# Optimization experiments

Hardware: AMD Instinct MI355X
Metric: run time of the kernel (lower is better)

Reference implementation:

```python
import jax, jax.numpy as jnp
import numpy as np

N_AGENTS = 10000
N_TARGETS = 10000
N_EDGES = 320000
IN_CH = 8
DS = 32          # n_channels // 2 per GAT preprocessor
NCH = 64         # n_channels
C = 128          # 2 * n_channels hidden width
OUT = 2
N_TAPS = 3
N_LAYERS = 2
RADIUS = 2.0
K_NBR = 10       # max_num_neighbors in radius_graph
BIG = 1e9


def radius_nbrs(qpos, kpos, radius, k, exclude_self):
    """For each query point, indices of <=k nearest key points within radius."""
    d2 = jnp.sum((qpos[:, None, :] - kpos[None, :, :]) ** 2, axis=-1)  # [Nq, Nk]
    if exclude_self:
        n = qpos.shape[0]
        d2 = d2.at[jnp.arange(n), jnp.arange(n)].set(BIG)
    d2 = jnp.where(d2 <= radius * radius, d2, BIG)
    negv, idx = jax.lax.top_k(-d2, k)   # nearest-k (deterministic stand-in for PyG's first-k)
    valid = negv > -BIG * 0.5           # [Nq, k] True where a real in-radius neighbor
    return idx, valid


def gatv2(src_feats, dst_feats, idx, valid, Wl, Wr, att, b):
    """Single-head GATv2Conv over a fixed-K neighbor list (idx indexes src_feats)."""
    xl = src_feats @ Wl                      # [Ns, H] messages
    xr = dst_feats @ Wr                      # [Nd, H]
    g = jax.nn.leaky_relu(xl[idx] + xr[:, None, :], 0.2)   # [Nd, K, H]
    s = jnp.einsum('nkh,h->nk', g, att)
    s = jnp.where(valid, s, -BIG)
    s = s - jnp.max(s, axis=1, keepdims=True)
    p = jnp.exp(s) * valid                   # masked exp; isolated nodes -> all-zero
    alpha = p / (jnp.sum(p, axis=1, keepdims=True) + 1e-16)
    return jnp.einsum('nk,nkh->nh', alpha, xl[idx]) + b


def graph_filter(x, src, dst, W, b, n):
    """Polynomial graph filter: y = sum_k S^k x W_k + b, S = unweighted adjacency."""
    y = x @ W[0]
    h = x
    for k in range(1, W.shape[0]):
        h = jax.ops.segment_sum(h[src], dst, num_segments=n)  # one shift tap
        y = y + h @ W[k]
    return y + b


def setup_inputs() -> dict:
    key = jax.random.key(0)
    ks = jax.random.split(key, 16)
    f32 = jnp.float32
    return {
        'own_obs': jax.random.normal(ks[0], (N_AGENTS, IN_CH), dtype=f32),
        'agent_positions': jax.random.uniform(ks[1], (N_AGENTS, 2), dtype=f32) * 100.0,
        'target_positions': jax.random.uniform(ks[2], (N_TARGETS, 2), dtype=f32) * 100.0,
        'W_self': jax.random.normal(ks[3], (IN_CH, NCH), dtype=f32) * 0.1,
        'b_self': jnp.zeros((NCH,), f32),
        'ag_Wl': jax.random.normal(ks[4], (2, DS), dtype=f32) * 0.1,
        'ag_Wr': jax.random.normal(ks[5], (2, DS), dtype=f32) * 0.1,
        'ag_att': jax.random.normal(ks[6], (DS,), dtype=f32) * 0.1,
        'ag_b': jnp.zeros((DS,), f32),
        'tg_Wl': jax.random.normal(ks[7], (2, DS), dtype=f32) * 0.1,
        'tg_Wr': jax.random.normal(ks[8], (2, DS), dtype=f32) * 0.1,
        'tg_att': jax.random.normal(ks[9], (DS,), dtype=f32) * 0.1,
        'tg_b': jnp.zeros((DS,), f32),
        'gf_W': jax.random.normal(ks[10], (N_LAYERS, N_TAPS + 1, C, C), dtype=f32) * (1.0 / np.sqrt(C)),
        'gf_b': jnp.zeros((N_LAYERS, C), f32),
        'bn_gamma': jnp.ones((N_LAYERS, C), f32),
        'bn_beta': jnp.zeros((N_LAYERS, C), f32),
        'W_read': jax.random.normal(ks[11], (C, OUT), dtype=f32) * 0.1,
        'b_read': jnp.zeros((OUT,), f32),
        'edge_index': jax.random.randint(ks[12], (2, N_EDGES), 0, N_AGENTS, dtype=jnp.int32),
    }


def reference(own_obs, agent_positions, target_positions, W_self, b_self,
              ag_Wl, ag_Wr, ag_att, ag_b, tg_Wl, tg_Wr, tg_att, tg_b,
              gf_W, gf_b, bn_gamma, bn_beta, W_read, b_read, edge_index):
    n = agent_positions.shape[0]
    # dynamic radius graphs (agent-agent; target->agent)
    a_idx, a_valid = radius_nbrs(agent_positions, agent_positions, RADIUS, K_NBR, True)
    t_idx, t_valid = radius_nbrs(agent_positions, target_positions, RADIUS, K_NBR, False)

    s = own_obs @ W_self + b_self                                            # self MLP (1 layer)
    a = gatv2(agent_positions, agent_positions, a_idx, a_valid, ag_Wl, ag_Wr, ag_att, ag_b)
    t = gatv2(target_positions, agent_positions, t_idx, t_valid, tg_Wl, tg_Wr, tg_att, tg_b)
    x = jnp.concatenate([s, a, t], axis=1)                                   # [N, 128]

    src, dst = edge_index[0], edge_index[1]
    for l in range(N_LAYERS):
        h = graph_filter(x, src, dst, gf_W[l], gf_b[l], n)
        mu = jnp.mean(h, axis=0)
        var = jnp.var(h, axis=0)
        h = (h - mu) / jnp.sqrt(var + 1e-5) * bn_gamma[l] + bn_beta[l]       # BatchNorm
        x = x + jax.nn.leaky_relu(h, 0.01)                                   # residual block
    return x @ W_read + b_read
```

## Files before the change

### kernel.cpp

```cpp
#include <hip/hip_runtime.h>

typedef unsigned long long u64;
typedef unsigned int u32;
typedef unsigned short ushort_t;

#define NA 10000
#define NE 320000
#define KN 10
#define GRID 50
#define NCELL (GRID * GRID)

typedef __attribute__((ext_vector_type(8))) short short8v;
typedef __attribute__((ext_vector_type(4))) float f32x4;

__device__ __forceinline__ u32 f2bf(float f) {
  union { float f; u32 u; } v; v.f = f;
  return (v.u + 0x7fffu + ((v.u >> 16) & 1u)) >> 16;
}
__device__ __forceinline__ float bf2f(u32 b) {
  union { u32 u; float f; } v; v.u = b << 16;
  return v.f;
}

__device__ __forceinline__ void insert10(u64* top, u64 key) {
#pragma unroll
  for (int t = 9; t > 0; --t) {
    u64 prev = top[t - 1];
    u64 cur = top[t];
    top[t] = (key < prev) ? prev : ((key < cur) ? key : cur);
  }
  top[0] = (key < top[0]) ? key : top[0];
}

__device__ __forceinline__ int cell_of(float2 p) {
  int cx = (int)(p.x * 0.5f);
  int cy = (int)(p.y * 0.5f);
  cx = min(max(cx, 0), GRID - 1);
  cy = min(max(cy, 0), GRID - 1);
  return cy * GRID + cx;
}

__global__ __launch_bounds__(256) void k_zero_packw(int* __restrict__ deg, int* __restrict__ cur,
                                                    int* __restrict__ chist, int* __restrict__ ccur,
                                                    int* __restrict__ dcur,
                                                    const float* __restrict__ gfW,
                                                    ushort_t* __restrict__ Wh, ushort_t* __restrict__ Wlo) {
  int i = blockIdx.x * 256 + threadIdx.x;
  if (i < NA) deg[i] = 0;
  else if (i < 2 * NA) cur[i - NA] = 0;
  else if (i < 2 * NA + 2 * NCELL) chist[i - 2 * NA] = 0;
  else if (i < 2 * NA + 4 * NCELL) ccur[i - 2 * NA - 2 * NCELL] = 0;
  else if (i < 2 * NA + 4 * NCELL + 128) dcur[i - 2 * NA - 4 * NCELL] = 0;
  if (i < 131072) {
    int l = i >> 16;
    int rem = i & 65535;
    int t = rem >> 14;
    int k = (rem >> 7) & 127;
    int n = rem & 127;
    float v = gfW[(size_t)i];
    int kt = k >> 5;
    int hi = (k >> 3) & 3;
    int j = k & 7;
    int ct = n >> 4;
    int lane = hi * 16 + (n & 15);
    size_t dst = (((((size_t)(l * 4 + t) * 4 + kt) * 8 + ct) * 64 + lane) * 8 + j);
    u32 h = f2bf(v);
    float r = v - bf2f(h);
    Wh[dst] = (ushort_t)h;
    Wlo[dst] = (ushort_t)f2bf(r);
  }
}

__global__ __launch_bounds__(256) void k_hist_self(const int* __restrict__ edst,
                                                   const float2* __restrict__ apos,
                                                   const float2* __restrict__ tpos,
                                                   int* __restrict__ deg, int* __restrict__ chist,
                                                   const float* __restrict__ own_obs,
                                                   const float* __restrict__ W_self, const float* __restrict__ b_self,
                                                   float* __restrict__ x) {
  __shared__ float sW[512], sb[64];
  int t = threadIdx.x;
  for (int i = t; i < 512; i += 256) sW[i] = W_self[i];
  if (t < 64) sb[t] = b_self[t];
  __syncthreads();
  int i = blockIdx.x * 256 + t;
  if (i < NE) {
    atomicAdd(&deg[edst[i]], 1);
  } else if (i < NE + 2 * NA) {
    int ii = i - NE;
    int graph = (ii >= NA) ? 1 : 0;
    int idx = ii - graph * NA;
    float2 p = graph ? tpos[idx] : apos[idx];
    atomicAdd(&chist[graph * NCELL + cell_of(p)], 1);
  } else if (i < NE + 2 * NA + 8 * NA) {
    int gid = i - NE - 2 * NA;
    int q = gid >> 3;
    int c8 = (gid & 7) * 8;
    const float4* op = (const float4*)(own_obs + (size_t)q * 8);
    float4 o0 = op[0], o1 = op[1];
    float obs[8] = {o0.x, o0.y, o0.z, o0.w, o1.x, o1.y, o1.z, o1.w};
    float out[8];
#pragma unroll
    for (int jj = 0; jj < 8; ++jj) {
      int c = c8 + jj;
      float s = sb[c];
#pragma unroll
      for (int k = 0; k < 8; ++k) s += obs[k] * sW[k * 64 + c];
      out[jj] = s;
    }
    float* xrow = x + (size_t)q * 128 + c8;
    *(float4*)(xrow) = make_float4(out[0], out[1], out[2], out[3]);
    *(float4*)(xrow + 4) = make_float4(out[4], out[5], out[6], out[7]);
  }
}

__global__ __launch_bounds__(1024) void k_scan_all(const int* __restrict__ deg, int* __restrict__ rp,
                                                   const int* __restrict__ chist, int* __restrict__ crp,
                                                   int* __restrict__ dbase) {
  int t = threadIdx.x;
  if (blockIdx.x == 2) {
    __shared__ int dh[128];
    if (t < 128) dh[t] = 0;
    __syncthreads();
    for (int i = t; i < NA; i += 1024) atomicAdd(&dh[min(deg[i], 127)], 1);
    __syncthreads();
    if (t == 0) {
      int run = 0;
      for (int b = 0; b < 128; ++b) { int c = dh[b]; dbase[b] = run; run += c; }
    }
    return;
  }
  __shared__ int part[1024];
  const int* in;
  int* out;
  int per, tot;
  if (blockIdx.x == 0) { in = deg; out = rp; per = 10; tot = NA; }
  else { in = chist; out = crp; per = 5; tot = 2 * NCELL; }
  int beg = min(t * per, tot), end = min(beg + per, tot);
  int s = 0;
  for (int i = beg; i < end; ++i) s += in[i];
  part[t] = s;
  __syncthreads();
  for (int o = 1; o < 1024; o <<= 1) {
    int v = part[t];
    int u = (t >= o) ? part[t - o] : 0;
    __syncthreads();
    part[t] = v + u;
    __syncthreads();
  }
  int base = (t > 0) ? part[t - 1] : 0;
  for (int i = beg; i < end; ++i) { out[i] = base; base += in[i]; }
  if (t == 1023) out[tot] = part[1023];
}

__global__ __launch_bounds__(256) void k_scatter_all(const int* __restrict__ esrc, const int* __restrict__ edst,
                                                     const int* __restrict__ rp, int* __restrict__ cur,
                                                     int* __restrict__ col,
                                                     const float2* __restrict__ apos, const float2* __restrict__ tpos,
                                                     const int* __restrict__ crp, int* __restrict__ ccur,
                                                     float2* __restrict__ ps, int* __restrict__ pid,
                                                     const int* __restrict__ deg, const int* __restrict__ dbase,
                                                     int* __restrict__ dcur, int* __restrict__ perm) {
  int i = blockIdx.x * 256 + threadIdx.x;
  if (i < NE) {
    int d = edst[i];
    int p = atomicAdd(&cur[d], 1);
    col[rp[d] + p] = esrc[i];
  } else if (i < NE + 2 * NA) {
    int ii = i - NE;
    int graph = (ii >= NA) ? 1 : 0;
    int idx = ii - graph * NA;
    float2 p = graph ? tpos[idx] : apos[idx];
    int gc = graph * NCELL + cell_of(p);
    int o = crp[gc] + atomicAdd(&ccur[gc], 1);
    ps[o] = p;
    pid[o] = idx;
  } else if (i < NE + 2 * NA + NA) {
    int r = i - NE - 2 * NA;
    int b = min(deg[r], 127);
    int pos = atomicAdd(&dcur[b], 1);
    perm[dbase[b] + pos] = r;
  }
}

__global__ __launch_bounds__(256) void k_nbr_gat(const float2* __restrict__ apos, const float2* __restrict__ tpos,
                                                 const int* __restrict__ crp,
                                                 const float2* __restrict__ ps, const int* __restrict__ pid,
                                                 const float* __restrict__ agWl, const float* __restrict__ agWr,
                                                 const float* __restrict__ agatt, const float* __restrict__ agb,
                                                 const float* __restrict__ tgWl, const float* __restrict__ tgWr,
                                                 const float* __restrict__ tgatt, const float* __restrict__ tgb,
                                                 float* __restrict__ x) {
  __shared__ float sWl[2][64], sWr[2][64], satt[2][32], sbb[2][32];
  int t = threadIdx.x;
  if (t < 64) { sWl[0][t] = agWl[t]; sWr[0][t] = agWr[t]; sWl[1][t] = tgWl[t]; sWr[1][t] = tgWr[t]; }
  else if (t < 96) {
    int u = t - 64;
    satt[0][u] = agatt[u]; sbb[0][u] = agb[u]; satt[1][u] = tgatt[u]; sbb[1][u] = tgb[u];
  }
  __syncthreads();
  int tid = blockIdx.x * 256 + t;
  if (tid >= 2 * NA) return;
  int graph = (tid >= NA) ? 1 : 0;
  int q = tid - graph * NA;
  float2 qp = apos[q];
  int cx = min(max((int)(qp.x * 0.5f), 0), GRID - 1);
  int cy = min(max((int)(qp.y * 0.5f), 0), GRID - 1);

  u64 top[10];
#pragma unroll
  for (int k = 0; k < 10; ++k) top[k] = ~0ull;

  int x0 = max(cx - 1, 0), x1 = min(cx + 1, GRID - 1);
  int y0 = max(cy - 1, 0), y1 = min(cy + 1, GRID - 1);
  for (int yy = y0; yy <= y1; ++yy) {
    int cb = graph * NCELL + yy * GRID + x0;
    int ce = graph * NCELL + yy * GRID + x1;
    int b = crp[cb], e = crp[ce + 1];
    for (int j = b; j < e; ++j) {
      float2 kp = ps[j];
      float dx = qp.x - kp.x;
      float dy = qp.y - kp.y;
      float d2 = __fadd_rn(__fmul_rn(dx, dx), __fmul_rn(dy, dy));
      int g = pid[j];
      if (d2 <= 4.0f && !(graph == 0 && g == q)) {
        u64 key = ((u64)__float_as_uint(d2) << 32) | (u32)g;
        if (key < top[9]) insert10(top, key);
      }
    }
  }
  int cnt = 0;
#pragma unroll
  for (int k = 0; k < 10; ++k) cnt += (top[k] != ~0ull) ? 1 : 0;
  int idx[10];
#pragma unroll
  for (int k = 0; k < 10; ++k) idx[k] = (k < cnt) ? (int)(u32)(top[k] & 0xffffffffu) : 0;

  const float2* srcpos = graph ? tpos : apos;
  const float* wl = sWl[graph];
  const float* wr = sWr[graph];
  const float* at = satt[graph];
  const float* bb = sbb[graph];
  float xr[32];
#pragma unroll
  for (int c = 0; c < 32; ++c) xr[c] = qp.x * wr[c] + qp.y * wr[32 + c];
  float pv[10];
  float m = -1e30f;
#pragma unroll
  for (int k = 0; k < 10; ++k) {
    float2 p = srcpos[idx[k]];
    float s = 0.f;
#pragma unroll
    for (int c = 0; c < 32; ++c) {
      float xl = p.x * wl[c] + p.y * wl[32 + c];
      float g = xl + xr[c];
      g = (g >= 0.f) ? g : 0.2f * g;
      s += at[c] * g;
    }
    pv[k] = s;
    m = (k < cnt) ? fmaxf(m, s) : m;
  }
  float sum = 0.f;
#pragma unroll
  for (int k = 0; k < 10; ++k) {
    float e = (k < cnt) ? expf(pv[k] - m) : 0.f;
    pv[k] = e;
    sum += e;
  }
  float inv = 1.f / (sum + 1e-16f);
  float out[32];
#pragma unroll
  for (int c = 0; c < 32; ++c) out[c] = bb[c];
#pragma unroll
  for (int k = 0; k < 10; ++k) {
    float a = pv[k] * inv;
    float2 p = srcpos[idx[k]];
#pragma unroll
    for (int c = 0; c < 32; ++c) {
      float xl = p.x * wl[c] + p.y * wl[32 + c];
      out[c] += a * xl;
    }
  }
  float* xrow = x + (size_t)q * 128 + (graph ? 96 : 64);
#pragma unroll
  for (int c4 = 0; c4 < 8; ++c4)
    *(float4*)(xrow + c4 * 4) = make_float4(out[c4 * 4], out[c4 * 4 + 1], out[c4 * 4 + 2], out[c4 * 4 + 3]);
}

__global__ __launch_bounds__(256) void k_shift3(const float* __restrict__ xin, float* __restrict__ xout,
                                                const int* __restrict__ rp, const int* __restrict__ col,
                                                const int* __restrict__ perm) {
  int bid = blockIdx.x;
  int half = (bid & 7) >> 2;
  int slot = (bid >> 3) * 4 + (bid & 3);
  if (slot >= 625) return;
  int wid = threadIdx.x >> 6;
  int lane = threadIdx.x & 63;
  int q = lane >> 4;
  int li = lane & 15;
  int row = perm[slot * 16 + wid * 4 + q];
  int beg = rp[row], end = rp[row + 1];
  const f32x4* x4 = (const f32x4*)xin;
  int base = half * 16 + li;
  f32x4 acc = {0.f, 0.f, 0.f, 0.f};
  int j = beg;
  for (; j + 3 < end; j += 4) {
    int s0 = col[j], s1 = col[j + 1], s2 = col[j + 2], s3 = col[j + 3];
    f32x4 v0 = x4[(size_t)s0 * 32 + base];
    f32x4 v1 = x4[(size_t)s1 * 32 + base];
    f32x4 v2 = x4[(size_t)s2 * 32 + base];
    f32x4 v3 = x4[(size_t)s3 * 32 + base];
    acc += v0;
    acc += v1;
    acc += v2;
    acc += v3;
  }
  for (; j < end; ++j) acc += x4[(size_t)col[j] * 32 + base];
  __builtin_nontemporal_store(acc, &((f32x4*)xout)[(size_t)row * 32 + base]);
}

__global__ __launch_bounds__(256) void k_gemm_mfma3(const float* __restrict__ a0, const float* __restrict__ a1,
                                                    const float* __restrict__ a2, const float* __restrict__ a3,
                                                    const ushort_t* __restrict__ Wh, const ushort_t* __restrict__ Wlo,
                                                    const float* __restrict__ b, float* __restrict__ y,
                                                    double* __restrict__ parts) {
  const int lane = threadIdx.x & 63;
  const int wave = threadIdx.x >> 6;
  const int ct0 = wave * 2;
  const int row = lane & 15;
  const int hi = lane >> 4;
  const int rb = blockIdx.x * 16;

  f32x4 acc[2];
#pragma unroll
  for (int c = 0; c < 2; ++c) {
    float bv = b[(ct0 + c) * 16 + row];
    acc[c][0] = bv; acc[c][1] = bv; acc[c][2] = bv; acc[c][3] = bv;
  }

  const float* aps[4] = {a0, a1, a2, a3};
#pragma unroll
  for (int t = 0; t < 4; ++t) {
    const float* at = aps[t];
#pragma unroll
    for (int kt = 0; kt < 4; ++kt) {
      const float* ap = at + (size_t)(rb + row) * 128 + kt * 32 + hi * 8;
      float4 fa = *(const float4*)(ap);
      float4 fb = *(const float4*)(ap + 4);
      float av[8] = {fa.x, fa.y, fa.z, fa.w, fb.x, fb.y, fb.z, fb.w};
      short8v ah, al;
#pragma unroll
      for (int j = 0; j < 8; ++j) {
        u32 h = f2bf(av[j]);
        float r = av[j] - bf2f(h);
        ah[j] = (short)h;
        al[j] = (short)f2bf(r);
      }
#pragma unroll
      for (int c = 0; c < 2; ++c) {
        size_t widx = ((((size_t)t * 4 + kt) * 8 + (ct0 + c)) * 64 + lane) * 8;
        short8v bh = *(const short8v*)(Wh + widx);
        short8v bl = *(const short8v*)(Wlo + widx);
        acc[c] = __builtin_amdgcn_mfma_f32_16x16x32_bf16(ah, bh, acc[c], 0, 0, 0);
        acc[c] = __builtin_amdgcn_mfma_f32_16x16x32_bf16(al, bh, acc[c], 0, 0, 0);
        acc[c] = __builtin_amdgcn_mfma_f32_16x16x32_bf16(ah, bl, acc[c], 0, 0, 0);
      }
    }
  }

#pragma unroll
  for (int c = 0; c < 2; ++c) {
#pragma unroll
    for (int r = 0; r < 4; ++r) {
      int grow = rb + hi * 4 + r;
      y[(size_t)grow * 128 + (ct0 + c) * 16 + row] = acc[c][r];
    }
  }

#pragma unroll
  for (int c = 0; c < 2; ++c) {
    double s = 0.0, ss = 0.0;
#pragma unroll
    for (int r = 0; r < 4; ++r) {
      double v = (double)acc[c][r];
      s += v;
      ss += v * v;
    }
    s += __shfl_xor(s, 16);
    ss += __shfl_xor(ss, 16);
    s += __shfl_xor(s, 32);
    ss += __shfl_xor(ss, 32);
    if (hi == 0) {
      int ch = (ct0 + c) * 16 + row;
      parts[(size_t)ch * 625 + blockIdx.x] = s;
      parts[(size_t)(128 + ch) * 625 + blockIdx.x] = ss;
    }
  }
}

__global__ __launch_bounds__(256) void k_bnfin(const double* __restrict__ parts,
                                               const float* __restrict__ gamma, const float* __restrict__ beta,
                                               float* __restrict__ AB) {
  __shared__ double s0[256], s1[256];
  int ch = blockIdx.x;
  int t = threadIdx.x;
  const double* ps = parts + (size_t)ch * 625;
  const double* pq = parts + (size_t)(128 + ch) * 625;
  double a = 0.0, b = 0.0;
  for (int i = t; i < 625; i += 256) { a += ps[i]; b += pq[i]; }
  s0[t] = a;
  s1[t] = b;
  __syncthreads();
  for (int o = 128; o > 0; o >>= 1) {
    if (t < o) { s0[t] += s0[t + o]; s1[t] += s1[t + o]; }
    __syncthreads();
  }
  if (t == 0) {
    double mu = s0[0] / (double)NA;
    double var = s1[0] / (double)NA - mu * mu;
    double rs = 1.0 / sqrt(var + 1e-5);
    AB[ch] = (float)rs * gamma[ch];
    AB[128 + ch] = beta[ch] - (float)(mu * rs) * gamma[ch];
  }
}

__global__ __launch_bounds__(256) void k_bnapply(const float* __restrict__ y, const float* __restrict__ AB,
                                                 const float* __restrict__ Wread, const float* __restrict__ bread,
                                                 float* __restrict__ x, float* __restrict__ out, int doread) {
  __shared__ float sAB[256], sWr[256];
  int t = threadIdx.x;
  sAB[t] = AB[t];
  sWr[t] = Wread[t];
  __syncthreads();
  const int n4 = NA * 32;
  for (int i = blockIdx.x * 256 + t; i < n4; i += gridDim.x * 256) {
    float4 yv = ((const float4*)y)[i];
    int c = (i & 31) * 4;
    float v0 = yv.x * sAB[c + 0] + sAB[128 + c + 0];
    float v1 = yv.y * sAB[c + 1] + sAB[128 + c + 1];
    float v2 = yv.z * sAB[c + 2] + sAB[128 + c + 2];
    float v3 = yv.w * sAB[c + 3] + sAB[128 + c + 3];
    v0 = (v0 >= 0.f) ? v0 : 0.01f * v0;
    v1 = (v1 >= 0.f) ? v1 : 0.01f * v1;
    v2 = (v2 >= 0.f) ? v2 : 0.01f * v2;
    v3 = (v3 >= 0.f) ? v3 : 0.01f * v3;
    float4 xv = ((float4*)x)[i];
    xv.x += v0; xv.y += v1; xv.z += v2; xv.w += v3;
    ((float4*)x)[i] = xv;
    if (doread) {
      float a0 = xv.x * sWr[(c + 0) * 2] + xv.y * sWr[(c + 1) * 2] + xv.z * sWr[(c + 2) * 2] + xv.w * sWr[(c + 3) * 2];
      float a1 = xv.x * sWr[(c + 0) * 2 + 1] + xv.y * sWr[(c + 1) * 2 + 1] + xv.z * sWr[(c + 2) * 2 + 1] + xv.w * sWr[(c + 3) * 2 + 1];
#pragma unroll
      for (int o = 1; o < 32; o <<= 1) {
        a0 += __shfl_xor(a0, o);
        a1 += __shfl_xor(a1, o);
      }
      if ((i & 31) == 0) {
        int row = i >> 5;
        out[row * 2 + 0] = a0 + bread[0];
        out[row * 2 + 1] = a1 + bread[1];
      }
    }
  }
}

extern "C" void kernel_launch(void* const* d_in, const int* in_sizes, int n_in,
                              void* d_out, int out_size, void* d_ws, size_t ws_size,
                              hipStream_t stream) {
  (void)in_sizes; (void)n_in; (void)out_size; (void)ws_size;
  const float* own_obs = (const float*)d_in[0];
  const float2* apos = (const float2*)d_in[1];
  const float2* tpos = (const float2*)d_in[2];
  const float* W_self = (const float*)d_in[3];
  const float* b_self = (const float*)d_in[4];
  const float* agWl = (const float*)d_in[5];
  const float* agWr = (const float*)d_in[6];
  const float* agatt = (const float*)d_in[7];
  const float* agb = (const float*)d_in[8];
  const float* tgWl = (const float*)d_in[9];
  const float* tgWr = (const float*)d_in[10];
  const float* tgatt = (const float*)d_in[11];
  const float* tgb = (const float*)d_in[12];
  const float* gfW = (const float*)d_in[13];
  const float* gfb = (const float*)d_in[14];
  const float* bng = (const float*)d_in[15];
  const float* bnb = (const float*)d_in[16];
  const float* Wread = (const float*)d_in[17];
  const float* bread = (const float*)d_in[18];
  const int* ei = (const int*)d_in[19];
  const int* esrc = ei;
  const int* edst = ei + NE;

  char* w = (char*)d_ws;
  size_t off = 0;
  auto take = [&](size_t bytes) -> void* {
    void* p = w + off;
    off += (bytes + 255) & ~(size_t)255;
    return p;
  };
  float* x = (float*)take((size_t)NA * 128 * 4);
  float* y = (float*)take((size_t)NA * 128 * 4);
  float* sh1 = (float*)take((size_t)NA * 128 * 4);
  float* sh2 = (float*)take((size_t)NA * 128 * 4);
  float* sh3 = (float*)take((size_t)NA * 128 * 4);
  ushort_t* Wh = (ushort_t*)take((size_t)131072 * 2);
  ushort_t* Wlo = (ushort_t*)take((size_t)131072 * 2);
  double* parts = (double*)take((size_t)256 * 625 * 8);
  float* AB = (float*)take(256 * 4);
  int* deg = (int*)take((size_t)NA * 4);
  int* cur = (int*)take((size_t)NA * 4);
  int* rp = (int*)take((size_t)(NA + 1) * 4);
  int* col = (int*)take((size_t)NE * 4);
  int* chist = (int*)take((size_t)2 * NCELL * 4);
  int* crp = (int*)take((size_t)(2 * NCELL + 1) * 4);
  int* ccur = (int*)take((size_t)2 * NCELL * 4);
  float2* ps = (float2*)take((size_t)2 * NA * 8);
  int* pid = (int*)take((size_t)2 * NA * 4);
  int* dbase = (int*)take(128 * 4);
  int* dcur = (int*)take(128 * 4);
  int* perm = (int*)take((size_t)NA * 4);

  k_zero_packw<<<131072 / 256, 256, 0, stream>>>(deg, cur, chist, ccur, dcur, gfW, Wh, Wlo);
  k_hist_self<<<(NE + 2 * NA + 8 * NA + 255) / 256, 256, 0, stream>>>(edst, apos, tpos, deg, chist,
                                                                      own_obs, W_self, b_self, x);
  k_scan_all<<<3, 1024, 0, stream>>>(deg, rp, chist, crp, dbase);
  k_scatter_all<<<(NE + 3 * NA + 255) / 256, 256, 0, stream>>>(esrc, edst, rp, cur, col,
                                                               apos, tpos, crp, ccur, ps, pid,
                                                               deg, dbase, dcur, perm);
  k_nbr_gat<<<(2 * NA + 255) / 256, 256, 0, stream>>>(apos, tpos, crp, ps, pid,
                                                      agWl, agWr, agatt, agb, tgWl, tgWr, tgatt, tgb, x);

  for (int l = 0; l < 2; ++l) {
    const ushort_t* Whl = Wh + (size_t)l * 65536;
    const ushort_t* Wll = Wlo + (size_t)l * 65536;
    const float* bl = gfb + (size_t)l * 128;
    const float* gl = bng + (size_t)l * 128;
    const float* bb = bnb + (size_t)l * 128;
    k_shift3<<<1256, 256, 0, stream>>>(x, sh1, rp, col, perm);
    k_shift3<<<1256, 256, 0, stream>>>(sh1, sh2, rp, col, perm);
    k_shift3<<<1256, 256, 0, stream>>>(sh2, sh3, rp, col, perm);
    k_gemm_mfma3<<<NA / 16, 256, 0, stream>>>(x, sh1, sh2, sh3, Whl, Wll, bl, y, parts);
    k_bnfin<<<128, 256, 0, stream>>>(parts, gl, bb, AB);
    k_bnapply<<<256, 256, 0, stream>>>(y, AB, Wread, bread, x, (float*)d_out, l == 1 ? 1 : 0);
  }
}
```

Before: 254.4 us.

## Drop degree-sorted row permutation, fold weight packing into hist kernel, use memset

Removes the degree-bucket permutation (histogram, scan block, scatter) and the separate zero/pack kernel. Zeroing now uses one hipMemsetAsync over reordered contiguous buffers, and the weight bf16 split-packing is merged into k_hist_self. The SpMM shift kernel is rewritten to use half-waves per row with float2 loads in natural row order. This cuts setup kernels and the perm indirection, at the cost of possible load imbalance across rows of different degree.

```diff
diff --git a/kernel.cpp b/kernel.cpp
--- a/kernel.cpp
+++ b/kernel.cpp
@@ -40,44 +40,15 @@
   return cy * GRID + cx;
 }
 
-__global__ __launch_bounds__(256) void k_zero_packw(int* __restrict__ deg, int* __restrict__ cur,
-                                                    int* __restrict__ chist, int* __restrict__ ccur,
-                                                    int* __restrict__ dcur,
-                                                    const float* __restrict__ gfW,
-                                                    ushort_t* __restrict__ Wh, ushort_t* __restrict__ Wlo) {
-  int i = blockIdx.x * 256 + threadIdx.x;
-  if (i < NA) deg[i] = 0;
-  else if (i < 2 * NA) cur[i - NA] = 0;
-  else if (i < 2 * NA + 2 * NCELL) chist[i - 2 * NA] = 0;
-  else if (i < 2 * NA + 4 * NCELL) ccur[i - 2 * NA - 2 * NCELL] = 0;
-  else if (i < 2 * NA + 4 * NCELL + 128) dcur[i - 2 * NA - 4 * NCELL] = 0;
-  if (i < 131072) {
-    int l = i >> 16;
-    int rem = i & 65535;
-    int t = rem >> 14;
-    int k = (rem >> 7) & 127;
-    int n = rem & 127;
-    float v = gfW[(size_t)i];
-    int kt = k >> 5;
-    int hi = (k >> 3) & 3;
-    int j = k & 7;
-    int ct = n >> 4;
-    int lane = hi * 16 + (n & 15);
-    size_t dst = (((((size_t)(l * 4 + t) * 4 + kt) * 8 + ct) * 64 + lane) * 8 + j);
-    u32 h = f2bf(v);
-    float r = v - bf2f(h);
-    Wh[dst] = (ushort_t)h;
-    Wlo[dst] = (ushort_t)f2bf(r);
-  }
-}
-
 __global__ __launch_bounds__(256) void k_hist_self(const int* __restrict__ edst,
                                                    const float2* __restrict__ apos,
                                                    const float2* __restrict__ tpos,
                                                    int* __restrict__ deg, int* __restrict__ chist,
                                                    const float* __restrict__ own_obs,
                                                    const float* __restrict__ W_self, const float* __restrict__ b_self,
-                                                   float* __restrict__ x) {
+                                                   float* __restrict__ x,
+                                                   const float* __restrict__ gfW,
+                                                   ushort_t* __restrict__ Wh, ushort_t* __restrict__ Wlo) {
   __shared__ float sW[512], sb[64];
   int t = threadIdx.x;
   for (int i = t; i < 512; i += 256) sW[i] = W_self[i];
@@ -111,26 +82,31 @@
     float* xrow = x + (size_t)q * 128 + c8;
     *(float4*)(xrow) = make_float4(out[0], out[1], out[2], out[3]);
     *(float4*)(xrow + 4) = make_float4(out[4], out[5], out[6], out[7]);
+  } else if (i < NE + 2 * NA + 8 * NA + 131072) {
+    int w = i - NE - 2 * NA - 8 * NA;
+    int l = w >> 16;
+    int rem = w & 65535;
+    int tt = rem >> 14;
+    int k = (rem >> 7) & 127;
+    int n = rem & 127;
+    float v = gfW[(size_t)w];
+    int kt = k >> 5;
+    int hi = (k >> 3) & 3;
+    int j = k & 7;
+    int ct = n >> 4;
+    int lane = hi * 16 + (n & 15);
+    size_t dst = (((((size_t)(l * 4 + tt) * 4 + kt) * 8 + ct) * 64 + lane) * 8 + j);
+    u32 h = f2bf(v);
+    float r = v - bf2f(h);
+    Wh[dst] = (ushort_t)h;
+    Wlo[dst] = (ushort_t)f2bf(r);
   }
 }
 
 __global__ __launch_bounds__(1024) void k_scan_all(const int* __restrict__ deg, int* __restrict__ rp,
-                                                   const int* __restrict__ chist, int* __restrict__ crp,
-                                                   int* __restrict__ dbase) {
+                                                   const int* __restrict__ chist, int* __restrict__ crp) {
+  __shared__ int part[1024];
   int t = threadIdx.x;
-  if (blockIdx.x == 2) {
-    __shared__ int dh[128];
-    if (t < 128) dh[t] = 0;
-    __syncthreads();
-    for (int i = t; i < NA; i += 1024) atomicAdd(&dh[min(deg[i], 127)], 1);
-    __syncthreads();
-    if (t == 0) {
-      int run = 0;
-      for (int b = 0; b < 128; ++b) { int c = dh[b]; dbase[b] = run; run += c; }
-    }
-    return;
-  }
-  __shared__ int part[1024];
   const int* in;
   int* out;
   int per, tot;
@@ -158,9 +134,7 @@
                                                      int* __restrict__ col,
                                                      const float2* __restrict__ apos, const float2* __restrict__ tpos,
                                                      const int* __restrict__ crp, int* __restrict__ ccur,
-                                                     float2* __restrict__ ps, int* __restrict__ pid,
-                                                     const int* __restrict__ deg, const int* __restrict__ dbase,
-                                                     int* __restrict__ dcur, int* __restrict__ perm) {
+                                                     float2* __restrict__ ps, int* __restrict__ pid) {
   int i = blockIdx.x * 256 + threadIdx.x;
   if (i < NE) {
     int d = edst[i];
@@ -175,11 +149,6 @@
     int o = crp[gc] + atomicAdd(&ccur[gc], 1);
     ps[o] = p;
     pid[o] = idx;
-  } else if (i < NE + 2 * NA + NA) {
-    int r = i - NE - 2 * NA;
-    int b = min(deg[r], 127);
-    int pos = atomicAdd(&dcur[b], 1);
-    perm[dbase[b] + pos] = r;
   }
 }
 
@@ -287,36 +256,36 @@
     *(float4*)(xrow + c4 * 4) = make_float4(out[c4 * 4], out[c4 * 4 + 1], out[c4 * 4 + 2], out[c4 * 4 + 3]);
 }
 
-__global__ __launch_bounds__(256) void k_shift3(const float* __restrict__ xin, float* __restrict__ xout,
-                                                const int* __restrict__ rp, const int* __restrict__ col,
-                                                const int* __restrict__ perm) {
+__global__ __launch_bounds__(256) void k_shift4(const float* __restrict__ xin, float* __restrict__ xout,
+                                                const int* __restrict__ rp, const int* __restrict__ col) {
   int bid = blockIdx.x;
   int half = (bid & 7) >> 2;
   int slot = (bid >> 3) * 4 + (bid & 3);
-  if (slot >= 625) return;
-  int wid = threadIdx.x >> 6;
-  int lane = threadIdx.x & 63;
-  int q = lane >> 4;
-  int li = lane & 15;
-  int row = perm[slot * 16 + wid * 4 + q];
+  if (slot >= 1250) return;
+  int hw = threadIdx.x >> 5;
+  int li = threadIdx.x & 31;
+  int row = slot * 8 + hw;
   int beg = rp[row], end = rp[row + 1];
-  const f32x4* x4 = (const f32x4*)xin;
-  int base = half * 16 + li;
-  f32x4 acc = {0.f, 0.f, 0.f, 0.f};
+  const float2* x2 = (const float2*)xin;
+  int base = half * 32 + li;
+  float2 acc = {0.f, 0.f};
   int j = beg;
   for (; j + 3 < end; j += 4) {
     int s0 = col[j], s1 = col[j + 1], s2 = col[j + 2], s3 = col[j + 3];
-    f32x4 v0 = x4[(size_t)s0 * 32 + base];
-    f32x4 v1 = x4[(size_t)s1 * 32 + base];
-    f32x4 v2 = x4[(size_t)s2 * 32 + base];
-    f32x4 v3 = x4[(size_t)s3 * 32 + base];
-    acc += v0;
-    acc += v1;
-    acc += v2;
-    acc += v3;
-  }
-  for (; j < end; ++j) acc += x4[(size_t)col[j] * 32 + base];
-  __builtin_nontemporal_store(acc, &((f32x4*)xout)[(size_t)row * 32 + base]);
+    float2 v0 = x2[(size_t)s0 * 64 + base];
+    float2 v1 = x2[(size_t)s1 * 64 + base];
+    float2 v2 = x2[(size_t)s2 * 64 + base];
+    float2 v3 = x2[(size_t)s3 * 64 + base];
+    acc.x += v0.x; acc.y += v0.y;
+    acc.x += v1.x; acc.y += v1.y;
+    acc.x += v2.x; acc.y += v2.y;
+    acc.x += v3.x; acc.y += v3.y;
+  }
+  for (; j < end; ++j) {
+    float2 v = x2[(size_t)col[j] * 64 + base];
+    acc.x += v.x; acc.y += v.y;
+  }
+  ((float2*)xout)[(size_t)row * 64 + base] = acc;
 }
 
 __global__ __launch_bounds__(256) void k_gemm_mfma3(const float* __restrict__ a0, const float* __restrict__ a1,
@@ -509,24 +478,20 @@
   float* AB = (float*)take(256 * 4);
   int* deg = (int*)take((size_t)NA * 4);
   int* cur = (int*)take((size_t)NA * 4);
+  int* chist = (int*)take((size_t)2 * NCELL * 4);
+  int* ccur = (int*)take((size_t)2 * NCELL * 4);
   int* rp = (int*)take((size_t)(NA + 1) * 4);
   int* col = (int*)take((size_t)NE * 4);
-  int* chist = (int*)take((size_t)2 * NCELL * 4);
   int* crp = (int*)take((size_t)(2 * NCELL + 1) * 4);
-  int* ccur = (int*)take((size_t)2 * NCELL * 4);
   float2* ps = (float2*)take((size_t)2 * NA * 8);
   int* pid = (int*)take((size_t)2 * NA * 4);
-  int* dbase = (int*)take(128 * 4);
-  int* dcur = (int*)take(128 * 4);
-  int* perm = (int*)take((size_t)NA * 4);
-
-  k_zero_packw<<<131072 / 256, 256, 0, stream>>>(deg, cur, chist, ccur, dcur, gfW, Wh, Wlo);
-  k_hist_self<<<(NE + 2 * NA + 8 * NA + 255) / 256, 256, 0, stream>>>(edst, apos, tpos, deg, chist,
-                                                                      own_obs, W_self, b_self, x);
-  k_scan_all<<<3, 1024, 0, stream>>>(deg, rp, chist, crp, dbase);
-  k_scatter_all<<<(NE + 3 * NA + 255) / 256, 256, 0, stream>>>(esrc, edst, rp, cur, col,
-                                                               apos, tpos, crp, ccur, ps, pid,
-                                                               deg, dbase, dcur, perm);
+
+  hipMemsetAsync(deg, 0, (size_t)((char*)(ccur + 2 * NCELL) - (char*)deg), stream);
+  k_hist_self<<<(NE + 2 * NA + 8 * NA + 131072 + 255) / 256, 256, 0, stream>>>(
+      edst, apos, tpos, deg, chist, own_obs, W_self, b_self, x, gfW, Wh, Wlo);
+  k_scan_all<<<2, 1024, 0, stream>>>(deg, rp, chist, crp);
+  k_scatter_all<<<(NE + 2 * NA + 255) / 256, 256, 0, stream>>>(esrc, edst, rp, cur, col,
+                                                               apos, tpos, crp, ccur, ps, pid);
   k_nbr_gat<<<(2 * NA + 255) / 256, 256, 0, stream>>>(apos, tpos, crp, ps, pid,
                                                       agWl, agWr, agatt, agb, tgWl, tgWr, tgatt, tgb, x);
 
@@ -536,9 +501,9 @@
     const float* bl = gfb + (size_t)l * 128;
     const float* gl = bng + (size_t)l * 128;
     const float* bb = bnb + (size_t)l * 128;
-    k_shift3<<<1256, 256, 0, stream>>>(x, sh1, rp, col, perm);
-    k_shift3<<<1256, 256, 0, stream>>>(sh1, sh2, rp, col, perm);
-    k_shift3<<<1256, 256, 0, stream>>>(sh2, sh3, rp, col, perm);
+    k_shift4<<<2504, 256, 0, stream>>>(x, sh1, rp, col);
+    k_shift4<<<2504, 256, 0, stream>>>(sh1, sh2, rp, col);
+    k_shift4<<<2504, 256, 0, stream>>>(sh2, sh3, rp, col);
     k_gemm_mfma3<<<NA / 16, 256, 0, stream>>>(x, sh1, sh2, sh3, Whl, Wll, bl, y, parts);
     k_bnfin<<<128, 256, 0, stream>>>(parts, gl, bb, AB);
     k_bnapply<<<256, 256, 0, stream>>>(y, AB, Wread, bread, x, (float*)d_out, l == 1 ? 1 : 0);
```

Result: slower. 280.5 us (+10.3%).
